# Optimization experiments

Hardware: AMD Instinct MI355X
Metric: run time of the kernel (lower is better)

Reference implementation:

```python
import jax, jax.numpy as jnp
import numpy as np

# (H, W, D) per level; flatten index within a level is z*H*W + y*W + x (z-major)
SPATIAL_SHAPES = [(32, 32, 32), (16, 16, 16), (8, 8, 8), (4, 4, 4)]
N, LQ, DM, NH, NL, NP = 1, 4000, 256, 8, 4, 4
DH = DM // NH
LEN_IN = sum(h * w * d for h, w, d in SPATIAL_SHAPES)  # 37440


def setup_inputs() -> dict:
    key = jax.random.key(0)
    ks = jax.random.split(key, 8)
    s = 0.02
    return {
        "query": jax.random.normal(ks[0], (N, LQ, DM), jnp.float32),
        "reference_points": jax.random.uniform(ks[1], (N, LQ, NL, 3), jnp.float32),
        "input_flatten": jax.random.normal(ks[2], (N, LEN_IN, DM), jnp.float32),
        "w_value": jax.random.normal(ks[3], (DM, DM), jnp.float32) * s,
        "b_value": jnp.zeros((DM,), jnp.float32),
        "w_off": jax.random.normal(ks[4], (DM, NH * NL * NP * 3), jnp.float32) * s,
        "b_off": jnp.zeros((NH * NL * NP * 3,), jnp.float32),
        "w_attn": jax.random.normal(ks[5], (DM, NH * NL * NP), jnp.float32) * s,
        "b_attn": jnp.zeros((NH * NL * NP,), jnp.float32),
        "w_out": jax.random.normal(ks[6], (DM, DM), jnp.float32) * s,
        "b_out": jnp.zeros((DM,), jnp.float32),
    }


def ms_deform_attn_core(value, sampling_locations, attention_weights):
    """value [N,Len_in,NH,DH]; loc [N,LQ,NH,NL,NP,3] (x,y,z in [0,1]);
    attn [N,LQ,NH,NL,NP]. Trilinear sampling, zero padding, align_corners=False."""
    n, lq = sampling_locations.shape[:2]
    out = jnp.zeros((n, lq, NH, DH), value.dtype)
    start = 0
    for lvl, (H, W, D) in enumerate(SPATIAL_SHAPES):
        L = H * W * D
        v = value[:, start:start + L]                 # [N, L, NH, DH]
        loc = sampling_locations[:, :, :, lvl]        # [N, LQ, NH, NP, 3]
        aw = attention_weights[:, :, :, lvl]          # [N, LQ, NH, NP]
        x = loc[..., 0] * W - 0.5
        y = loc[..., 1] * H - 0.5
        z = loc[..., 2] * D - 0.5
        x0f, y0f, z0f = jnp.floor(x), jnp.floor(y), jnp.floor(z)
        fx, fy, fz = x - x0f, y - y0f, z - z0f
        x0, y0, z0 = x0f.astype(jnp.int32), y0f.astype(jnp.int32), z0f.astype(jnp.int32)
        for dz in (0, 1):
            wz = fz if dz else 1.0 - fz
            for dy in (0, 1):
                wy = fy if dy else 1.0 - fy
                for dx in (0, 1):
                    wx = fx if dx else 1.0 - fx
                    xi, yi, zi = x0 + dx, y0 + dy, z0 + dz
                    valid = ((xi >= 0) & (xi < W) & (yi >= 0) & (yi < H)
                             & (zi >= 0) & (zi < D)).astype(value.dtype)
                    cw = wx * wy * wz * valid * aw    # [N, LQ, NH, NP]
                    idx = (jnp.clip(zi, 0, D - 1) * (H * W)
                           + jnp.clip(yi, 0, H - 1) * W
                           + jnp.clip(xi, 0, W - 1))  # [N, LQ, NH, NP]
                    idxr = idx.transpose(0, 1, 3, 2).reshape(n, lq * NP, NH)[..., None]
                    g = jnp.take_along_axis(v, idxr, axis=1).reshape(n, lq, NP, NH, DH)
                    out = out + jnp.einsum('nqphd,nqhp->nqhd', g, cw)
        start += L
    return out


def reference(query, reference_points, input_flatten, w_value, b_value,
              w_off, b_off, w_attn, b_attn, w_out, b_out):
    n, lq, _ = query.shape
    value = (input_flatten @ w_value + b_value).reshape(n, -1, NH, DH)
    off = (query @ w_off + b_off).reshape(n, lq, NH, NL, NP, 3)
    attn = jax.nn.softmax(
        (query @ w_attn + b_attn).reshape(n, lq, NH, NL * NP), axis=-1
    ).reshape(n, lq, NH, NL, NP)
    shapes = jnp.asarray(SPATIAL_SHAPES, jnp.float32)  # rows (H, W, D)
    # faithful to source: normalizer = stack([shapes[:,2], shapes[:,1], shapes[:,0]])
    normalizer = jnp.stack([shapes[:, 2], shapes[:, 1], shapes[:, 0]], -1)  # [NL, 3]
    loc = (reference_points[:, :, None, :, None, :]
           + off / normalizer[None, None, None, :, None, :])
    out = ms_deform_attn_core(value, loc, attn)
    return out.reshape(n, lq, DM) @ w_out + b_out
```

## Files before the change

kernel.cpp:

```cpp
#include <hip/hip_runtime.h>
#include <hip/hip_bf16.h>

#define NQ     4000
#define DMODEL 256
#define NHEAD  8
#define NLVL   4
#define NPT    4
#define DHEAD  32
#define LENIN  37440
#define NOFF   384
#define NATT   128
#define NPROJ  512

#define NVBLK  (LENIN / 64)
#define NQBLK  ((NQ + 63) / 64)
#define LDH    40
#define LDSW   132

typedef _Float16 f16x8 __attribute__((ext_vector_type(8)));
typedef _Float16 f16x4 __attribute__((ext_vector_type(4)));
typedef float    f32x4 __attribute__((ext_vector_type(4)));

__global__ __launch_bounds__(256) void cast_transpose_all(
    const float* __restrict__ wv, const float* __restrict__ wo,
    const float* __restrict__ wa, const float* __restrict__ wu,
    _Float16* __restrict__ wvT, _Float16* __restrict__ catT,
    _Float16* __restrict__ wuT)
{
    __shared__ float t[64][65];
    const int xt = blockIdx.x, kt = blockIdx.y;
    const float* W; _Float16* WT; int ncols, col0, nbase;
    if (xt < 4)       { W = wv; WT = wvT;  ncols = 256; col0 = xt * 64;        nbase = col0; }
    else if (xt < 10) { W = wo; WT = catT; ncols = 384; col0 = (xt - 4) * 64;  nbase = col0; }
    else if (xt < 12) { W = wa; WT = catT; ncols = 128; col0 = (xt - 10) * 64; nbase = 384 + col0; }
    else              { W = wu; WT = wuT;  ncols = 256; col0 = (xt - 12) * 64; nbase = col0; }

    const int by = kt * 64;
    const int tid = threadIdx.x;
    const int c = tid & 63, r0 = tid >> 6;
    #pragma unroll
    for (int i = 0; i < 16; ++i) {
        int r = r0 + i * 4;
        t[r][c] = W[(size_t)(by + r) * ncols + col0 + c];
    }
    __syncthreads();
    #pragma unroll
    for (int i = 0; i < 16; ++i) {
        int n = r0 + i * 4;
        WT[(size_t)(nbase + n) * DMODEL + by + c] = (_Float16)t[c][n];
    }
}

__global__ __launch_bounds__(256) void gemm_front(
    const float* __restrict__ Aval, const float* __restrict__ query,
    const _Float16* __restrict__ wvT, const _Float16* __restrict__ catT,
    const float* __restrict__ bval, const float* __restrict__ boff,
    const float* __restrict__ batt,
    _Float16* __restrict__ valueH, _Float16* __restrict__ proj)
{
    __shared__ __align__(16) char smem[25600];
    _Float16 (*As)[LDH] = (_Float16 (*)[LDH])smem;
    _Float16 (*Bs)[LDH] = (_Float16 (*)[LDH])(smem + 64 * LDH * 2);

    const int tid  = threadIdx.x;
    const int wave = tid >> 6, lane = tid & 63;
    const int l15 = lane & 15, l16 = lane >> 4;

    const int  bid   = blockIdx.x;
    const bool isval = (bid < NVBLK);
    const float* A; const _Float16* BT; int brow, ncb, M;
    if (isval) { A = Aval;  BT = wvT;  brow = bid * 64;  ncb = 0;  M = LENIN; }
    else       { int idx = bid - NVBLK; A = query; BT = catT;
                 brow = (idx >> 1) * 64; ncb = (idx & 1) * 256; M = NQ; }

    const int arow = tid >> 2, akq = (tid & 3) * 8;
    int arg = brow + arow; if (arg >= M) arg = M - 1;
    const float* aptr = A + (size_t)arg * DMODEL + akq;

    const _Float16* bptr[4];
    int bn[4], bkc[4];
    #pragma unroll
    for (int j = 0; j < 4; ++j) {
        int id = tid + 256 * j;
        bn[j] = id >> 2; bkc[j] = (id & 3) * 8;
        bptr[j] = BT + (size_t)(ncb + bn[j]) * DMODEL + bkc[j];
    }

    f32x4 acc[4][4] = {};
    float4 a0, a1;
    f16x8 bh[4];

    a0 = *(const float4*)(const void*)aptr;
    a1 = *(const float4*)(const void*)(aptr + 4);
    #pragma unroll
    for (int j = 0; j < 4; ++j) bh[j] = *(const f16x8*)bptr[j];

    for (int k0 = 0; k0 < DMODEL; k0 += 32) {
        {
            f16x8 h;
            h[0] = (_Float16)a0.x; h[1] = (_Float16)a0.y;
            h[2] = (_Float16)a0.z; h[3] = (_Float16)a0.w;
            h[4] = (_Float16)a1.x; h[5] = (_Float16)a1.y;
            h[6] = (_Float16)a1.z; h[7] = (_Float16)a1.w;
            *(f16x8*)&As[arow][akq] = h;
        }
        #pragma unroll
        for (int j = 0; j < 4; ++j) *(f16x8*)&Bs[bn[j]][bkc[j]] = bh[j];
        __syncthreads();

        if (k0 + 32 < DMODEL) {
            a0 = *(const float4*)(const void*)(aptr + k0 + 32);
            a1 = *(const float4*)(const void*)(aptr + k0 + 36);
            #pragma unroll
            for (int j = 0; j < 4; ++j) bh[j] = *(const f16x8*)(bptr[j] + k0 + 32);
        }

        f16x8 af[4], bf[4];
        #pragma unroll
        for (int mi = 0; mi < 4; ++mi)
            af[mi] = *(const f16x8*)&As[mi * 16 + l15][l16 * 8];
        #pragma unroll
        for (int ni = 0; ni < 4; ++ni)
            bf[ni] = *(const f16x8*)&Bs[wave * 64 + ni * 16 + l15][l16 * 8];
        #pragma unroll
        for (int mi = 0; mi < 4; ++mi)
            #pragma unroll
            for (int ni = 0; ni < 4; ++ni)
                acc[mi][ni] = __builtin_amdgcn_mfma_f32_16x16x32_f16(
                    af[mi], bf[ni], acc[mi][ni], 0, 0, 0);
        __syncthreads();
    }

    if (isval) {
        _Float16 (*out_s)[LDSW] = (_Float16 (*)[LDSW])smem;
        const int cell = tid >> 2, dchunk = tid & 3;
        #pragma unroll
        for (int hh = 0; hh < 2; ++hh) {
            if ((wave >> 1) == hh) {
                int cb = (wave & 1) * 64;
                #pragma unroll
                for (int ni = 0; ni < 4; ++ni) {
                    int col = wave * 64 + ni * 16 + l15;
                    float b = bval[col];
                    #pragma unroll
                    for (int mi = 0; mi < 4; ++mi)
                        #pragma unroll
                        for (int j = 0; j < 4; ++j)
                            out_s[mi * 16 + l16 * 4 + j][cb + ni * 16 + l15] =
                                (_Float16)(acc[mi][ni][j] + b);
                }
            }
            __syncthreads();
            #pragma unroll
            for (int h2 = 0; h2 < 4; ++h2) {
                int h = hh * 4 + h2;
                f16x4 lo = *(const f16x4*)&out_s[cell][h2 * 32 + dchunk * 8];
                f16x4 hi = *(const f16x4*)&out_s[cell][h2 * 32 + dchunk * 8 + 4];
                size_t base = ((size_t)h * LENIN + brow + cell) * DHEAD + dchunk * 8;
                *(f16x4*)&valueH[base]     = lo;
                *(f16x4*)&valueH[base + 4] = hi;
            }
            __syncthreads();
        }
    } else {
        #pragma unroll
        for (int ni = 0; ni < 4; ++ni) {
            int col = ncb + wave * 64 + ni * 16 + l15;
            float b = (col < NOFF) ? boff[col] : batt[col - NOFF];
            #pragma unroll
            for (int mi = 0; mi < 4; ++mi)
                #pragma unroll
                for (int j = 0; j < 4; ++j) {
                    int row = brow + mi * 16 + l16 * 4 + j;
                    if (row < NQ)
                        proj[(size_t)row * NPROJ + col] = (_Float16)(acc[mi][ni][j] + b);
                }
        }
    }
}

__global__ __launch_bounds__(256) void sample_fused4(
    const _Float16* __restrict__ value, const _Float16* __restrict__ proj,
    const float* __restrict__ refpts, _Float16* __restrict__ oat)
{
    __shared__ float    loc_s[4][NOFF];
    __shared__ float    aw_s[4][NATT];
    __shared__ unsigned ca_s[4][1056];
    __shared__ _Float16 cw_s[4][1056];

    const int tid  = threadIdx.x;
    const int wv   = tid >> 6, lane = tid & 63;
    const int q    = blockIdx.x * 4 + wv;
    const _Float16* pq = proj + (size_t)q * NPROJ;

    #pragma unroll
    for (int i = 0; i < 8; ++i) {
        int t = i * 64 + lane;
        float v = (float)pq[t];
        if (t < NOFF) {
            int t2 = t / 3, lvl = (t2 >> 2) & 3, c = t - t2 * 3;
            float norm = (float)(32 >> lvl);
            loc_s[wv][t] = refpts[((size_t)q * NLVL + lvl) * 3 + c] + v / norm;
        } else {
            float m = v;
            #pragma unroll
            for (int o = 8; o >= 1; o >>= 1) m = fmaxf(m, __shfl_xor(m, o, 16));
            float e = expf(v - m);
            float s = e;
            #pragma unroll
            for (int o = 8; o >= 1; o >>= 1) s += __shfl_xor(s, o, 16);
            aw_s[wv][t - NOFF] = e / s;
        }
    }
    __syncthreads();

    #pragma unroll
    for (int i = 0; i < 16; ++i) {
        int id = i * 64 + lane;
        int h = id >> 7, pt = (id >> 3) & 15, c = id & 7;
        int lvl = pt >> 2;
        int S = 32 >> lvl;
        float Sf = (float)S;
        int base = (lvl == 0) ? 0 : (lvl == 1) ? 32768 : (lvl == 2) ? 36864 : 37376;

        float lx = loc_s[wv][h * 48 + pt * 3 + 0];
        float ly = loc_s[wv][h * 48 + pt * 3 + 1];
        float lz = loc_s[wv][h * 48 + pt * 3 + 2];
        float aw = aw_s[wv][h * 16 + pt];

        float x = lx * Sf - 0.5f, y = ly * Sf - 0.5f, z = lz * Sf - 0.5f;
        float x0f = floorf(x), y0f = floorf(y), z0f = floorf(z);
        float fx = x - x0f, fy = y - y0f, fz = z - z0f;
        int dx = c & 1, dy = (c >> 1) & 1, dz = c >> 2;
        int xi = (int)x0f + dx, yi = (int)y0f + dy, zi = (int)z0f + dz;
        float wx = dx ? fx : 1.f - fx;
        float wy = dy ? fy : 1.f - fy;
        float wz = dz ? fz : 1.f - fz;
        bool valid = (unsigned)xi < (unsigned)S &&
                     (unsigned)yi < (unsigned)S &&
                     (unsigned)zi < (unsigned)S;
        int idx = (zi * S + yi) * S + xi;
        unsigned addr = valid ? (unsigned)(h * LENIN + base + idx) * 64u
                              : (unsigned)(h * LENIN) * 64u;
        float w = valid ? wx * wy * wz * aw : 0.f;
        ca_s[wv][h * 132 + pt * 8 + c] = addr;
        cw_s[wv][h * 132 + pt * 8 + c] = (_Float16)w;
    }
    __syncthreads();

    const int h = lane >> 3, s = lane & 7;
    const int chunk = s & 3, half4 = (s >> 2) * 4;
    const char* vb = (const char*)value + chunk * 16;
    const unsigned* ca = &ca_s[wv][h * 132];
    const _Float16* cwp = &cw_s[wv][h * 132];

    float acc[8] = {};
    #pragma unroll 4
    for (int pt = 0; pt < 16; ++pt) {
        uint4 a4 = *(const uint4*)&ca[pt * 8 + half4];
        f16x4 w4 = *(const f16x4*)&cwp[pt * 8 + half4];
        {
            f16x8 v = *(const f16x8*)(vb + a4.x); float w = (float)w4[0];
            #pragma unroll
            for (int j = 0; j < 8; ++j) acc[j] += w * (float)v[j];
        }
        {
            f16x8 v = *(const f16x8*)(vb + a4.y); float w = (float)w4[1];
            #pragma unroll
            for (int j = 0; j < 8; ++j) acc[j] += w * (float)v[j];
        }
        {
            f16x8 v = *(const f16x8*)(vb + a4.z); float w = (float)w4[2];
            #pragma unroll
            for (int j = 0; j < 8; ++j) acc[j] += w * (float)v[j];
        }
        {
            f16x8 v = *(const f16x8*)(vb + a4.w); float w = (float)w4[3];
            #pragma unroll
            for (int j = 0; j < 8; ++j) acc[j] += w * (float)v[j];
        }
    }
    #pragma unroll
    for (int j = 0; j < 8; ++j) acc[j] += __shfl_xor(acc[j], 4);

    if (s < 4) {
        f16x8 r;
        #pragma unroll
        for (int j = 0; j < 8; ++j) r[j] = (_Float16)acc[j];
        *(f16x8*)&oat[(size_t)q * DMODEL + h * DHEAD + chunk * 8] = r;
    }
}

__global__ __launch_bounds__(256) void gemm_out(
    const _Float16* __restrict__ A, const _Float16* __restrict__ BT,
    const float* __restrict__ bias, float* __restrict__ C)
{
    __shared__ __align__(16) _Float16 As[64][LDH];
    __shared__ __align__(16) _Float16 Bs[128][LDH];
    const int tid  = threadIdx.x;
    const int wave = tid >> 6, lane = tid & 63;
    const int brow = blockIdx.x * 64;
    const int bcol = blockIdx.y * 128;
    const int l15 = lane & 15, l16 = lane >> 4;

    const int arow = tid >> 2, akq = (tid & 3) * 8;
    int arg = brow + arow; if (arg >= NQ) arg = NQ - 1;
    const _Float16* aptr = A + (size_t)arg * DMODEL + akq;

    const _Float16* bptr[2];
    int bn[2], bkc[2];
    #pragma unroll
    for (int j = 0; j < 2; ++j) {
        int id = tid + 256 * j;
        bn[j] = id >> 2; bkc[j] = (id & 3) * 8;
        bptr[j] = BT + (size_t)(bcol + bn[j]) * DMODEL + bkc[j];
    }

    f32x4 acc[4][2] = {};
    f16x8 ah, bh[2];
    ah = *(const f16x8*)(const void*)aptr;
    #pragma unroll
    for (int j = 0; j < 2; ++j) bh[j] = *(const f16x8*)bptr[j];

    for (int k0 = 0; k0 < DMODEL; k0 += 32) {
        *(f16x8*)&As[arow][akq] = ah;
        #pragma unroll
        for (int j = 0; j < 2; ++j) *(f16x8*)&Bs[bn[j]][bkc[j]] = bh[j];
        __syncthreads();

        if (k0 + 32 < DMODEL) {
            ah = *(const f16x8*)(const void*)(aptr + k0 + 32);
            #pragma unroll
            for (int j = 0; j < 2; ++j) bh[j] = *(const f16x8*)(bptr[j] + k0 + 32);
        }

        f16x8 af[4], bf[2];
        #pragma unroll
        for (int mi = 0; mi < 4; ++mi)
            af[mi] = *(const f16x8*)&As[mi * 16 + l15][l16 * 8];
        #pragma unroll
        for (int ni = 0; ni < 2; ++ni)
            bf[ni] = *(const f16x8*)&Bs[wave * 32 + ni * 16 + l15][l16 * 8];
        #pragma unroll
        for (int mi = 0; mi < 4; ++mi)
            #pragma unroll
            for (int ni = 0; ni < 2; ++ni)
                acc[mi][ni] = __builtin_amdgcn_mfma_f32_16x16x32_f16(
                    af[mi], bf[ni], acc[mi][ni], 0, 0, 0);
        __syncthreads();
    }

    #pragma unroll
    for (int ni = 0; ni < 2; ++ni) {
        int col = bcol + wave * 32 + ni * 16 + l15;
        float b = bias[col];
        #pragma unroll
        for (int mi = 0; mi < 4; ++mi)
            #pragma unroll
            for (int j = 0; j < 4; ++j) {
                int row = brow + mi * 16 + l16 * 4 + j;
                if (row < NQ)
                    C[(size_t)row * DMODEL + col] = acc[mi][ni][j] + b;
            }
    }
}

extern "C" void kernel_launch(void* const* d_in, const int* in_sizes, int n_in,
                              void* d_out, int out_size, void* d_ws, size_t ws_size,
                              hipStream_t stream) {
    const float* query         = (const float*)d_in[0];
    const float* refpts        = (const float*)d_in[1];
    const float* input_flatten = (const float*)d_in[2];
    const float* w_value       = (const float*)d_in[3];
    const float* b_value       = (const float*)d_in[4];
    const float* w_off         = (const float*)d_in[5];
    const float* b_off         = (const float*)d_in[6];
    const float* w_attn        = (const float*)d_in[7];
    const float* b_attn        = (const float*)d_in[8];
    const float* w_out         = (const float*)d_in[9];
    const float* b_out         = (const float*)d_in[10];

    _Float16* valueH = (_Float16*)d_ws;
    _Float16* wvT    = valueH + (size_t)LENIN * DMODEL;
    _Float16* catT   = wvT + 256 * 256;
    _Float16* wuT    = catT + 512 * 256;
    _Float16* proj   = wuT + 256 * 256;
    _Float16* oatH   = proj + (size_t)NQ * NPROJ;

    cast_transpose_all<<<dim3(16, 4), 256, 0, stream>>>(
        w_value, w_off, w_attn, w_out, wvT, catT, wuT);

    gemm_front<<<NVBLK + NQBLK * 2, 256, 0, stream>>>(
        input_flatten, query, wvT, catT, b_value, b_off, b_attn, valueH, proj);

    sample_fused4<<<NQ / 4, 256, 0, stream>>>(valueH, proj, refpts, oatH);

    gemm_out<<<dim3(NQBLK, 2), 256, 0, stream>>>(oatH, wuT, b_out, (float*)d_out);
}
```

Measured before the change: 63.57 us.

## Merge four kernels into one persistent cooperative kernel with grid syncs

Replaces the four separate launches (weight cast, front GEMM, sampling, output GEMM) with a single cooperative persistent kernel. Blocks loop over job indices for each stage and separate the stages with grid-wide syncs. The goal is to remove launch overhead and inter-kernel gaps. In exchange, the grid is capped at 512 blocks, occupancy is limited by the shared 33.5KB smem, each stage's work must be spread over fewer blocks, and the host now queries device properties on every call. A fallback path to the separate kernels is kept.

```diff
diff --git a/kernel.cpp b/kernel.cpp
--- a/kernel.cpp
+++ b/kernel.cpp
@@ -1,5 +1,8 @@
 #include <hip/hip_runtime.h>
 #include <hip/hip_bf16.h>
+#include <hip/hip_cooperative_groups.h>
+
+namespace cg = cooperative_groups;
 
 #define NQ     4000
 #define DMODEL 256
@@ -14,21 +17,25 @@
 
 #define NVBLK  (LENIN / 64)
 #define NQBLK  ((NQ + 63) / 64)
+#define NJF    (NVBLK + 2 * NQBLK)
+#define NJS    (NQ / 4)
+#define NJO    (2 * NQBLK)
 #define LDH    40
 #define LDSW   132
+#define SMEM_MAX 33536
 
 typedef _Float16 f16x8 __attribute__((ext_vector_type(8)));
 typedef _Float16 f16x4 __attribute__((ext_vector_type(4)));
 typedef float    f32x4 __attribute__((ext_vector_type(4)));
 
-__global__ __launch_bounds__(256) void cast_transpose_all(
+static __device__ void do_cast(int job, char* smem,
     const float* __restrict__ wv, const float* __restrict__ wo,
     const float* __restrict__ wa, const float* __restrict__ wu,
     _Float16* __restrict__ wvT, _Float16* __restrict__ catT,
     _Float16* __restrict__ wuT)
 {
-    __shared__ float t[64][65];
-    const int xt = blockIdx.x, kt = blockIdx.y;
+    float (*t)[65] = (float (*)[65])smem;
+    const int xt = job >> 2, kt = job & 3;
     const float* W; _Float16* WT; int ncols, col0, nbase;
     if (xt < 4)       { W = wv; WT = wvT;  ncols = 256; col0 = xt * 64;        nbase = col0; }
     else if (xt < 10) { W = wo; WT = catT; ncols = 384; col0 = (xt - 4) * 64;  nbase = col0; }
@@ -49,16 +56,16 @@
         int n = r0 + i * 4;
         WT[(size_t)(nbase + n) * DMODEL + by + c] = (_Float16)t[c][n];
     }
-}
-
-__global__ __launch_bounds__(256) void gemm_front(
+    __syncthreads();
+}
+
+static __device__ void do_front(int job, char* smem,
     const float* __restrict__ Aval, const float* __restrict__ query,
     const _Float16* __restrict__ wvT, const _Float16* __restrict__ catT,
     const float* __restrict__ bval, const float* __restrict__ boff,
     const float* __restrict__ batt,
     _Float16* __restrict__ valueH, _Float16* __restrict__ proj)
 {
-    __shared__ __align__(16) char smem[25600];
     _Float16 (*As)[LDH] = (_Float16 (*)[LDH])smem;
     _Float16 (*Bs)[LDH] = (_Float16 (*)[LDH])(smem + 64 * LDH * 2);
 
@@ -66,11 +73,10 @@
     const int wave = tid >> 6, lane = tid & 63;
     const int l15 = lane & 15, l16 = lane >> 4;
 
-    const int  bid   = blockIdx.x;
-    const bool isval = (bid < NVBLK);
+    const bool isval = (job < NVBLK);
     const float* A; const _Float16* BT; int brow, ncb, M;
-    if (isval) { A = Aval;  BT = wvT;  brow = bid * 64;  ncb = 0;  M = LENIN; }
-    else       { int idx = bid - NVBLK; A = query; BT = catT;
+    if (isval) { A = Aval;  BT = wvT;  brow = job * 64;  ncb = 0;  M = LENIN; }
+    else       { int idx = job - NVBLK; A = query; BT = catT;
                  brow = (idx >> 1) * 64; ncb = (idx & 1) * 256; M = NQ; }
 
     const int arow = tid >> 2, akq = (tid & 3) * 8;
@@ -176,21 +182,22 @@
                         proj[(size_t)row * NPROJ + col] = (_Float16)(acc[mi][ni][j] + b);
                 }
         }
-    }
-}
-
-__global__ __launch_bounds__(256) void sample_fused4(
+        __syncthreads();
+    }
+}
+
+static __device__ void do_sample(int job, char* smem,
     const _Float16* __restrict__ value, const _Float16* __restrict__ proj,
     const float* __restrict__ refpts, _Float16* __restrict__ oat)
 {
-    __shared__ float    loc_s[4][NOFF];
-    __shared__ float    aw_s[4][NATT];
-    __shared__ unsigned ca_s[4][1056];
-    __shared__ _Float16 cw_s[4][1056];
+    float*    loc_s = (float*)smem;
+    float*    aw_s  = (float*)(smem + 6144);
+    unsigned* ca_s  = (unsigned*)(smem + 8192);
+    _Float16* cw_s  = (_Float16*)(smem + 25088);
 
     const int tid  = threadIdx.x;
     const int wv   = tid >> 6, lane = tid & 63;
-    const int q    = blockIdx.x * 4 + wv;
+    const int q    = job * 4 + wv;
     const _Float16* pq = proj + (size_t)q * NPROJ;
 
     #pragma unroll
@@ -200,7 +207,7 @@
         if (t < NOFF) {
             int t2 = t / 3, lvl = (t2 >> 2) & 3, c = t - t2 * 3;
             float norm = (float)(32 >> lvl);
-            loc_s[wv][t] = refpts[((size_t)q * NLVL + lvl) * 3 + c] + v / norm;
+            loc_s[wv * NOFF + t] = refpts[((size_t)q * NLVL + lvl) * 3 + c] + v / norm;
         } else {
             float m = v;
             #pragma unroll
@@ -209,7 +216,7 @@
             float s = e;
             #pragma unroll
             for (int o = 8; o >= 1; o >>= 1) s += __shfl_xor(s, o, 16);
-            aw_s[wv][t - NOFF] = e / s;
+            aw_s[wv * NATT + (t - NOFF)] = e / s;
         }
     }
     __syncthreads();
@@ -223,10 +230,10 @@
         float Sf = (float)S;
         int base = (lvl == 0) ? 0 : (lvl == 1) ? 32768 : (lvl == 2) ? 36864 : 37376;
 
-        float lx = loc_s[wv][h * 48 + pt * 3 + 0];
-        float ly = loc_s[wv][h * 48 + pt * 3 + 1];
-        float lz = loc_s[wv][h * 48 + pt * 3 + 2];
-        float aw = aw_s[wv][h * 16 + pt];
+        float lx = loc_s[wv * NOFF + h * 48 + pt * 3 + 0];
+        float ly = loc_s[wv * NOFF + h * 48 + pt * 3 + 1];
+        float lz = loc_s[wv * NOFF + h * 48 + pt * 3 + 2];
+        float aw = aw_s[wv * NATT + h * 16 + pt];
 
         float x = lx * Sf - 0.5f, y = ly * Sf - 0.5f, z = lz * Sf - 0.5f;
         float x0f = floorf(x), y0f = floorf(y), z0f = floorf(z);
@@ -243,16 +250,16 @@
         unsigned addr = valid ? (unsigned)(h * LENIN + base + idx) * 64u
                               : (unsigned)(h * LENIN) * 64u;
         float w = valid ? wx * wy * wz * aw : 0.f;
-        ca_s[wv][h * 132 + pt * 8 + c] = addr;
-        cw_s[wv][h * 132 + pt * 8 + c] = (_Float16)w;
+        ca_s[wv * 1056 + h * 132 + pt * 8 + c] = addr;
+        cw_s[wv * 1056 + h * 132 + pt * 8 + c] = (_Float16)w;
     }
     __syncthreads();
 
     const int h = lane >> 3, s = lane & 7;
     const int chunk = s & 3, half4 = (s >> 2) * 4;
     const char* vb = (const char*)value + chunk * 16;
-    const unsigned* ca = &ca_s[wv][h * 132];
-    const _Float16* cwp = &cw_s[wv][h * 132];
+    const unsigned* ca  = &ca_s[wv * 1056 + h * 132];
+    const _Float16* cwp = &cw_s[wv * 1056 + h * 132];
 
     float acc[8] = {};
     #pragma unroll 4
@@ -289,18 +296,19 @@
         for (int j = 0; j < 8; ++j) r[j] = (_Float16)acc[j];
         *(f16x8*)&oat[(size_t)q * DMODEL + h * DHEAD + chunk * 8] = r;
     }
-}
-
-__global__ __launch_bounds__(256) void gemm_out(
+    __syncthreads();
+}
+
+static __device__ void do_out(int job, char* smem,
     const _Float16* __restrict__ A, const _Float16* __restrict__ BT,
     const float* __restrict__ bias, float* __restrict__ C)
 {
-    __shared__ __align__(16) _Float16 As[64][LDH];
-    __shared__ __align__(16) _Float16 Bs[128][LDH];
+    _Float16 (*As)[LDH] = (_Float16 (*)[LDH])smem;
+    _Float16 (*Bs)[LDH] = (_Float16 (*)[LDH])(smem + 64 * LDH * 2);
     const int tid  = threadIdx.x;
     const int wave = tid >> 6, lane = tid & 63;
-    const int brow = blockIdx.x * 64;
-    const int bcol = blockIdx.y * 128;
+    const int brow = (job >> 1) * 64;
+    const int bcol = (job & 1) * 128;
     const int l15 = lane & 15, l16 = lane >> 4;
 
     const int arow = tid >> 2, akq = (tid & 3) * 8;
@@ -363,6 +371,66 @@
                     C[(size_t)row * DMODEL + col] = acc[mi][ni][j] + b;
             }
     }
+    __syncthreads();
+}
+
+__global__ __launch_bounds__(256, 2) void mega(
+    const float* query, const float* refpts, const float* input_flatten,
+    const float* w_value, const float* b_value, const float* w_off,
+    const float* b_off, const float* w_attn, const float* b_attn,
+    const float* w_out, const float* b_out,
+    _Float16* valueH, _Float16* wvT, _Float16* catT, _Float16* wuT,
+    _Float16* proj, _Float16* oatH, float* out)
+{
+    __shared__ __align__(16) char smem[SMEM_MAX];
+    cg::grid_group grid = cg::this_grid();
+    const int b = blockIdx.x, G = gridDim.x;
+
+    for (int j = b; j < 64; j += G)
+        do_cast(j, smem, w_value, w_off, w_attn, w_out, wvT, catT, wuT);
+    __threadfence(); grid.sync();
+
+    for (int j = b; j < NJF; j += G)
+        do_front(j, smem, input_flatten, query, wvT, catT,
+                 b_value, b_off, b_attn, valueH, proj);
+    __threadfence(); grid.sync();
+
+    for (int j = b; j < NJS; j += G)
+        do_sample(j, smem, valueH, proj, refpts, oatH);
+    __threadfence(); grid.sync();
+
+    for (int j = b; j < NJO; j += G)
+        do_out(j, smem, oatH, wuT, b_out, out);
+}
+
+__global__ __launch_bounds__(256) void k_cast(
+    const float* wv, const float* wo, const float* wa, const float* wu,
+    _Float16* wvT, _Float16* catT, _Float16* wuT)
+{
+    __shared__ __align__(16) char smem[16640];
+    do_cast(blockIdx.x, smem, wv, wo, wa, wu, wvT, catT, wuT);
+}
+__global__ __launch_bounds__(256) void k_front(
+    const float* Aval, const float* query, const _Float16* wvT,
+    const _Float16* catT, const float* bval, const float* boff,
+    const float* batt, _Float16* valueH, _Float16* proj)
+{
+    __shared__ __align__(16) char smem[25600];
+    do_front(blockIdx.x, smem, Aval, query, wvT, catT, bval, boff, batt,
+             valueH, proj);
+}
+__global__ __launch_bounds__(256) void k_sample(
+    const _Float16* value, const _Float16* proj, const float* refpts,
+    _Float16* oat)
+{
+    __shared__ __align__(16) char smem[SMEM_MAX];
+    do_sample(blockIdx.x, smem, value, proj, refpts, oat);
+}
+__global__ __launch_bounds__(256) void k_out(
+    const _Float16* A, const _Float16* BT, const float* bias, float* C)
+{
+    __shared__ __align__(16) char smem[15360];
+    do_out(blockIdx.x, smem, A, BT, bias, C);
 }
 
 extern "C" void kernel_launch(void* const* d_in, const int* in_sizes, int n_in,
@@ -386,14 +454,36 @@
     _Float16* wuT    = catT + 512 * 256;
     _Float16* proj   = wuT + 256 * 256;
     _Float16* oatH   = proj + (size_t)NQ * NPROJ;
-
-    cast_transpose_all<<<dim3(16, 4), 256, 0, stream>>>(
-        w_value, w_off, w_attn, w_out, wvT, catT, wuT);
-
-    gemm_front<<<NVBLK + NQBLK * 2, 256, 0, stream>>>(
-        input_flatten, query, wvT, catT, b_value, b_off, b_attn, valueH, proj);
-
-    sample_fused4<<<NQ / 4, 256, 0, stream>>>(valueH, proj, refpts, oatH);
-
-    gemm_out<<<dim3(NQBLK, 2), 256, 0, stream>>>(oatH, wuT, b_out, (float*)d_out);
-}
+    float*    outp   = (float*)d_out;
+
+    int dev = 0;
+    hipGetDevice(&dev);
+    hipDeviceProp_t prop;
+    hipGetDeviceProperties(&prop, dev);
+    int maxb = 0;
+    if (hipOccupancyMaxActiveBlocksPerMultiprocessor(
+            &maxb, (const void*)mega, 256, 0) != hipSuccess || maxb <= 0)
+        maxb = 0;
+    int G = maxb * prop.multiProcessorCount;
+    if (G > 512) G = 512;
+
+    hipError_t cerr = hipErrorUnknown;
+    if (G >= 64) {
+        void* args[] = {
+            (void*)&query, (void*)&refpts, (void*)&input_flatten,
+            (void*)&w_value, (void*)&b_value, (void*)&w_off, (void*)&b_off,
+            (void*)&w_attn, (void*)&b_attn, (void*)&w_out, (void*)&b_out,
+            (void*)&valueH, (void*)&wvT, (void*)&catT, (void*)&wuT,
+            (void*)&proj, (void*)&oatH, (void*)&outp };
+        cerr = hipLaunchCooperativeKernel((const void*)mega, dim3(G), dim3(256),
+                                          args, 0, stream);
+    }
+    if (cerr != hipSuccess) {
+        k_cast<<<64, 256, 0, stream>>>(w_value, w_off, w_attn, w_out,
+                                       wvT, catT, wuT);
+        k_front<<<NJF, 256, 0, stream>>>(input_flatten, query, wvT, catT,
+                                         b_value, b_off, b_attn, valueH, proj);
+        k_sample<<<NJS, 256, 0, stream>>>(valueH, proj, refpts, oatH);
+        k_out<<<NJO, 256, 0, stream>>>(oatH, wuT, b_out, outp);
+    }
+}
```

New measurement: 82.70 us. 1.3x slower.

## Map sampling blocks to head×query-group and pack cell index with weight

Applied to the files above, without the earlier changes.

Restructures the sampling kernel so each block handles one head for 32 queries, and each wave handles 8 queries of that head. Within a wave, lanes split across the 16 points and 4 channel chunks and are reduced with a cross-lane shuffle tree. Each corner's cell index and fp16 weight are packed into one 32-bit shared-memory word. The aim is better cache locality, since blocks gather from a single head's value slab, and fewer shared-memory reads per corner. The cost is extra shuffle reductions, and the 16-bit cell index relies on per-level lengths fitting in 16 bits, which holds because the total is 37440.

```diff
diff --git a/kernel.cpp b/kernel.cpp
--- a/kernel.cpp
+++ b/kernel.cpp
@@ -179,29 +179,32 @@
     }
 }
 
-__global__ __launch_bounds__(256) void sample_fused4(
+__global__ __launch_bounds__(256) void sample_fused5(
     const _Float16* __restrict__ value, const _Float16* __restrict__ proj,
     const float* __restrict__ refpts, _Float16* __restrict__ oat)
 {
-    __shared__ float    loc_s[4][NOFF];
-    __shared__ float    aw_s[4][NATT];
-    __shared__ unsigned ca_s[4][1056];
-    __shared__ _Float16 cw_s[4][1056];
+    __shared__ float    loc_s[4][8][48];
+    __shared__ float    aw_s [4][8][16];
+    __shared__ unsigned cp_s [4][8][192];
 
     const int tid  = threadIdx.x;
     const int wv   = tid >> 6, lane = tid & 63;
-    const int q    = blockIdx.x * 4 + wv;
-    const _Float16* pq = proj + (size_t)q * NPROJ;
+    const int head = blockIdx.x & 7;
+    const int qg   = blockIdx.x >> 3;
+    const int q0   = qg * 32 + wv * 8;
 
     #pragma unroll
     for (int i = 0; i < 8; ++i) {
-        int t = i * 64 + lane;
-        float v = (float)pq[t];
-        if (t < NOFF) {
-            int t2 = t / 3, lvl = (t2 >> 2) & 3, c = t - t2 * 3;
+        const int q = q0 + i;
+        if (lane < 48) {
+            float v = (float)proj[(size_t)q * NPROJ + head * 48 + lane];
+            int pt = lane / 3, c = lane - pt * 3, lvl = pt >> 2;
             float norm = (float)(32 >> lvl);
-            loc_s[wv][t] = refpts[((size_t)q * NLVL + lvl) * 3 + c] + v / norm;
+            loc_s[wv][i][lane] =
+                refpts[((size_t)q * NLVL + lvl) * 3 + c] + v / norm;
         } else {
+            int j = lane - 48;
+            float v = (float)proj[(size_t)q * NPROJ + NOFF + head * 16 + j];
             float m = v;
             #pragma unroll
             for (int o = 8; o >= 1; o >>= 1) m = fmaxf(m, __shfl_xor(m, o, 16));
@@ -209,24 +212,24 @@
             float s = e;
             #pragma unroll
             for (int o = 8; o >= 1; o >>= 1) s += __shfl_xor(s, o, 16);
-            aw_s[wv][t - NOFF] = e / s;
+            aw_s[wv][i][j] = e / s;
         }
     }
     __syncthreads();
 
     #pragma unroll
-    for (int i = 0; i < 16; ++i) {
-        int id = i * 64 + lane;
-        int h = id >> 7, pt = (id >> 3) & 15, c = id & 7;
+    for (int k = 0; k < 16; ++k) {
+        int id = k * 64 + lane;
+        int i = id >> 7, pt = (id >> 3) & 15, c = id & 7;
         int lvl = pt >> 2;
         int S = 32 >> lvl;
         float Sf = (float)S;
         int base = (lvl == 0) ? 0 : (lvl == 1) ? 32768 : (lvl == 2) ? 36864 : 37376;
 
-        float lx = loc_s[wv][h * 48 + pt * 3 + 0];
-        float ly = loc_s[wv][h * 48 + pt * 3 + 1];
-        float lz = loc_s[wv][h * 48 + pt * 3 + 2];
-        float aw = aw_s[wv][h * 16 + pt];
+        float lx = loc_s[wv][i][pt * 3 + 0];
+        float ly = loc_s[wv][i][pt * 3 + 1];
+        float lz = loc_s[wv][i][pt * 3 + 2];
+        float aw = aw_s[wv][i][pt];
 
         float x = lx * Sf - 0.5f, y = ly * Sf - 0.5f, z = lz * Sf - 0.5f;
         float x0f = floorf(x), y0f = floorf(y), z0f = floorf(z);
@@ -240,54 +243,43 @@
                      (unsigned)yi < (unsigned)S &&
                      (unsigned)zi < (unsigned)S;
         int idx = (zi * S + yi) * S + xi;
-        unsigned addr = valid ? (unsigned)(h * LENIN + base + idx) * 64u
-                              : (unsigned)(h * LENIN) * 64u;
+        unsigned cell = valid ? (unsigned)(base + idx) : 0u;
         float w = valid ? wx * wy * wz * aw : 0.f;
-        ca_s[wv][h * 132 + pt * 8 + c] = addr;
-        cw_s[wv][h * 132 + pt * 8 + c] = (_Float16)w;
+        unsigned short wb = __builtin_bit_cast(unsigned short, (_Float16)w);
+        cp_s[wv][i][pt * 12 + c] = cell | ((unsigned)wb << 16);
     }
     __syncthreads();
 
-    const int h = lane >> 3, s = lane & 7;
-    const int chunk = s & 3, half4 = (s >> 2) * 4;
-    const char* vb = (const char*)value + chunk * 16;
-    const unsigned* ca = &ca_s[wv][h * 132];
-    const _Float16* cwp = &cw_s[wv][h * 132];
-
-    float acc[8] = {};
-    #pragma unroll 4
-    for (int pt = 0; pt < 16; ++pt) {
-        uint4 a4 = *(const uint4*)&ca[pt * 8 + half4];
-        f16x4 w4 = *(const f16x4*)&cwp[pt * 8 + half4];
-        {
-            f16x8 v = *(const f16x8*)(vb + a4.x); float w = (float)w4[0];
+    const int pt = lane >> 2, chunk = lane & 3;
+    const char* vb = (const char*)(value + (size_t)head * LENIN * DHEAD) + chunk * 16;
+
+    #pragma unroll
+    for (int i = 0; i < 8; ++i) {
+        const unsigned* cp = &cp_s[wv][i][pt * 12];
+        uint4 p0 = *(const uint4*)&cp[0];
+        uint4 p1 = *(const uint4*)&cp[4];
+
+        float acc[8] = {};
+        unsigned pk[8] = {p0.x, p0.y, p0.z, p0.w, p1.x, p1.y, p1.z, p1.w};
+        #pragma unroll
+        for (int c = 0; c < 8; ++c) {
+            unsigned p = pk[c];
+            float w = (float)__builtin_bit_cast(_Float16, (unsigned short)(p >> 16));
+            f16x8 v = *(const f16x8*)(vb + (size_t)(p & 0xFFFFu) * 64u);
             #pragma unroll
             for (int j = 0; j < 8; ++j) acc[j] += w * (float)v[j];
         }
-        {
-            f16x8 v = *(const f16x8*)(vb + a4.y); float w = (float)w4[1];
-            #pragma unroll
-            for (int j = 0; j < 8; ++j) acc[j] += w * (float)v[j];
-        }
-        {
-            f16x8 v = *(const f16x8*)(vb + a4.z); float w = (float)w4[2];
-            #pragma unroll
-            for (int j = 0; j < 8; ++j) acc[j] += w * (float)v[j];
-        }
-        {
-            f16x8 v = *(const f16x8*)(vb + a4.w); float w = (float)w4[3];
-            #pragma unroll
-            for (int j = 0; j < 8; ++j) acc[j] += w * (float)v[j];
-        }
-    }
-    #pragma unroll
-    for (int j = 0; j < 8; ++j) acc[j] += __shfl_xor(acc[j], 4);
-
-    if (s < 4) {
-        f16x8 r;
-        #pragma unroll
-        for (int j = 0; j < 8; ++j) r[j] = (_Float16)acc[j];
-        *(f16x8*)&oat[(size_t)q * DMODEL + h * DHEAD + chunk * 8] = r;
+        #pragma unroll
+        for (int o = 4; o <= 32; o <<= 1)
+            #pragma unroll
+            for (int j = 0; j < 8; ++j) acc[j] += __shfl_xor(acc[j], o);
+
+        if (pt == 0) {
+            f16x8 r;
+            #pragma unroll
+            for (int j = 0; j < 8; ++j) r[j] = (_Float16)acc[j];
+            *(f16x8*)&oat[(size_t)(q0 + i) * DMODEL + head * DHEAD + chunk * 8] = r;
+        }
     }
 }
 
@@ -393,7 +385,7 @@
     gemm_front<<<NVBLK + NQBLK * 2, 256, 0, stream>>>(
         input_flatten, query, wvT, catT, b_value, b_off, b_attn, valueH, proj);
 
-    sample_fused4<<<NQ / 4, 256, 0, stream>>>(valueH, proj, refpts, oatH);
+    sample_fused5<<<1000, 256, 0, stream>>>(valueH, proj, refpts, oatH);
 
     gemm_out<<<dim3(NQBLK, 2), 256, 0, stream>>>(oatH, wuT, b_out, (float*)d_out);
 }
```

Measured after the change: 70.21 us. +10.4%, slower.

## Remap sampling blocks to 16 queries by 2 heads for value locality

Applied to the files above, without the earlier changes.

The sampling kernel now gives each block 16 queries and a pair of heads, with blockIdx low bits picking the head pair, instead of 4 queries covering all 8 heads. The intent is to concentrate each block's gathers on two heads' slices of the value tensor, which should improve cache locality across blocks scheduled together. The per-head base offset is folded into the value pointer. The grid stays at 1000 blocks, and the corner-coordinate phase now loops over 16 queries per block, so per-thread setup work changes shape.

```diff
diff --git a/kernel.cpp b/kernel.cpp
--- a/kernel.cpp
+++ b/kernel.cpp
@@ -16,6 +16,7 @@
 #define NQBLK  ((NQ + 63) / 64)
 #define LDH    40
 #define LDSW   132
+#define CTB    132
 
 typedef _Float16 f16x8 __attribute__((ext_vector_type(8)));
 typedef _Float16 f16x4 __attribute__((ext_vector_type(4)));
@@ -179,54 +180,63 @@
     }
 }
 
-__global__ __launch_bounds__(256) void sample_fused4(
+__global__ __launch_bounds__(256) void sample_fused6(
     const _Float16* __restrict__ value, const _Float16* __restrict__ proj,
     const float* __restrict__ refpts, _Float16* __restrict__ oat)
 {
-    __shared__ float    loc_s[4][NOFF];
-    __shared__ float    aw_s[4][NATT];
-    __shared__ unsigned ca_s[4][1056];
-    __shared__ _Float16 cw_s[4][1056];
+    __shared__ float    loc_s[16][2][48];
+    __shared__ float    aw_s [16][2][16];
+    __shared__ unsigned ca_s [32 * CTB];
+    __shared__ _Float16 cw_s [32 * CTB];
 
     const int tid  = threadIdx.x;
     const int wv   = tid >> 6, lane = tid & 63;
-    const int q    = blockIdx.x * 4 + wv;
-    const _Float16* pq = proj + (size_t)q * NPROJ;
-
-    #pragma unroll
-    for (int i = 0; i < 8; ++i) {
-        int t = i * 64 + lane;
-        float v = (float)pq[t];
-        if (t < NOFF) {
-            int t2 = t / 3, lvl = (t2 >> 2) & 3, c = t - t2 * 3;
-            float norm = (float)(32 >> lvl);
-            loc_s[wv][t] = refpts[((size_t)q * NLVL + lvl) * 3 + c] + v / norm;
-        } else {
-            float m = v;
-            #pragma unroll
-            for (int o = 8; o >= 1; o >>= 1) m = fmaxf(m, __shfl_xor(m, o, 16));
-            float e = expf(v - m);
-            float s = e;
-            #pragma unroll
-            for (int o = 8; o >= 1; o >>= 1) s += __shfl_xor(s, o, 16);
-            aw_s[wv][t - NOFF] = e / s;
-        }
+    const int hp   = blockIdx.x & 3;
+    const int q0   = (blockIdx.x >> 2) * 16;
+
+    #pragma unroll
+    for (int it = 0; it < 6; ++it) {
+        int id = it * 256 + tid;
+        int lq = id / 96, r = id - lq * 96;
+        int h1 = r / 48,  c = r - h1 * 48;
+        int pt = c / 3,   ax = c - pt * 3, lvl = pt >> 2;
+        int head = hp * 2 + h1;
+        int q = q0 + lq;
+        float v = (float)proj[(size_t)q * NPROJ + head * 48 + c];
+        float norm = (float)(32 >> lvl);
+        loc_s[lq][h1][c] = refpts[((size_t)q * NLVL + lvl) * 3 + ax] + v / norm;
+    }
+    #pragma unroll
+    for (int it = 0; it < 2; ++it) {
+        int id = it * 256 + tid;
+        int lq = id >> 5, h1 = (id >> 4) & 1, j = id & 15;
+        int head = hp * 2 + h1;
+        int q = q0 + lq;
+        float v = (float)proj[(size_t)q * NPROJ + NOFF + head * 16 + j];
+        float m = v;
+        #pragma unroll
+        for (int o = 8; o >= 1; o >>= 1) m = fmaxf(m, __shfl_xor(m, o, 16));
+        float e = expf(v - m);
+        float s = e;
+        #pragma unroll
+        for (int o = 8; o >= 1; o >>= 1) s += __shfl_xor(s, o, 16);
+        aw_s[lq][h1][j] = e / s;
     }
     __syncthreads();
 
     #pragma unroll
-    for (int i = 0; i < 16; ++i) {
-        int id = i * 64 + lane;
-        int h = id >> 7, pt = (id >> 3) & 15, c = id & 7;
+    for (int k = 0; k < 16; ++k) {
+        const int lq = k;
+        int h1 = tid >> 7, pt = (tid >> 3) & 15, c = tid & 7;
         int lvl = pt >> 2;
         int S = 32 >> lvl;
         float Sf = (float)S;
         int base = (lvl == 0) ? 0 : (lvl == 1) ? 32768 : (lvl == 2) ? 36864 : 37376;
 
-        float lx = loc_s[wv][h * 48 + pt * 3 + 0];
-        float ly = loc_s[wv][h * 48 + pt * 3 + 1];
-        float lz = loc_s[wv][h * 48 + pt * 3 + 2];
-        float aw = aw_s[wv][h * 16 + pt];
+        float lx = loc_s[lq][h1][pt * 3 + 0];
+        float ly = loc_s[lq][h1][pt * 3 + 1];
+        float lz = loc_s[lq][h1][pt * 3 + 2];
+        float aw = aw_s[lq][h1][pt];
 
         float x = lx * Sf - 0.5f, y = ly * Sf - 0.5f, z = lz * Sf - 0.5f;
         float x0f = floorf(x), y0f = floorf(y), z0f = floorf(z);
@@ -240,19 +250,21 @@
                      (unsigned)yi < (unsigned)S &&
                      (unsigned)zi < (unsigned)S;
         int idx = (zi * S + yi) * S + xi;
-        unsigned addr = valid ? (unsigned)(h * LENIN + base + idx) * 64u
-                              : (unsigned)(h * LENIN) * 64u;
+        unsigned addr = valid ? (unsigned)(base + idx) * 64u : 0u;
         float w = valid ? wx * wy * wz * aw : 0.f;
-        ca_s[wv][h * 132 + pt * 8 + c] = addr;
-        cw_s[wv][h * 132 + pt * 8 + c] = (_Float16)w;
+        int g = lq * 2 + h1;
+        ca_s[g * CTB + pt * 8 + c] = addr;
+        cw_s[g * CTB + pt * 8 + c] = (_Float16)w;
     }
     __syncthreads();
 
-    const int h = lane >> 3, s = lane & 7;
+    const int q2 = (lane >> 4) & 3, h1 = (lane >> 3) & 1, s = lane & 7;
     const int chunk = s & 3, half4 = (s >> 2) * 4;
-    const char* vb = (const char*)value + chunk * 16;
-    const unsigned* ca = &ca_s[wv][h * 132];
-    const _Float16* cwp = &cw_s[wv][h * 132];
+    const int lq = wv * 4 + q2, g = lq * 2 + h1;
+    const int head = hp * 2 + h1;
+    const char* vb = (const char*)(value + (size_t)head * LENIN * DHEAD) + chunk * 16;
+    const unsigned* ca  = &ca_s[g * CTB];
+    const _Float16* cwp = &cw_s[g * CTB];
 
     float acc[8] = {};
     #pragma unroll 4
@@ -287,7 +299,7 @@
         f16x8 r;
         #pragma unroll
         for (int j = 0; j < 8; ++j) r[j] = (_Float16)acc[j];
-        *(f16x8*)&oat[(size_t)q * DMODEL + h * DHEAD + chunk * 8] = r;
+        *(f16x8*)&oat[(size_t)(q0 + lq) * DMODEL + head * DHEAD + chunk * 8] = r;
     }
 }
 
@@ -393,7 +405,7 @@
     gemm_front<<<NVBLK + NQBLK * 2, 256, 0, stream>>>(
         input_flatten, query, wvT, catT, b_value, b_off, b_attn, valueH, proj);
 
-    sample_fused4<<<NQ / 4, 256, 0, stream>>>(valueH, proj, refpts, oatH);
+    sample_fused6<<<1000, 256, 0, stream>>>(valueH, proj, refpts, oatH);
 
     gemm_out<<<dim3(NQBLK, 2), 256, 0, stream>>>(oatH, wuT, b_out, (float*)d_out);
 }
```

Measured after the change: 61.16 us. 3.8% less time.
